# Kernel tuning notes

Measured on AMD Instinct MI355X. Metric: run time of the kernel, lower is better.

## Reference

```python
import jax, jax.numpy as jnp
import numpy as np

BATCH = 256
SEQ_LEN = 512
INPUT_DIM = 1
NUM_HIDDEN = 2048
NUM_CLASSES = 10


def _xavier(key, shape):
    fan_out, fan_in = shape
    limit = np.sqrt(6.0 / (fan_in + fan_out)).astype(np.float32)
    return jax.random.uniform(key, shape, jnp.float32, -limit, limit)


def setup_inputs() -> dict:
    key = jax.random.key(0)
    kx, k1, k2, k3 = jax.random.split(key, 4)
    x = jax.random.normal(kx, (BATCH, SEQ_LEN), jnp.float32)
    wph = _xavier(k1, (NUM_CLASSES, NUM_HIDDEN))
    whh = _xavier(k2, (NUM_HIDDEN, NUM_HIDDEN))
    whx = _xavier(k3, (NUM_HIDDEN, INPUT_DIM))
    bh = jnp.zeros((NUM_HIDDEN,), jnp.float32)
    bp = jnp.zeros((NUM_CLASSES,), jnp.float32)
    return {"x": x, "whx": whx, "whh": whh, "bh": bh, "wph": wph, "bp": bp}


def reference(x, whx, whh, bh, wph, bp):
    # x: [B, T] of scalar inputs (input_dim == 1)
    B = x.shape[0]
    H = whh.shape[0]
    whx_vec = whx[:, 0]  # [H]

    def step(h, xt):
        # xt: [B];  xt[:, None] @ whx.T  ==  outer(xt, whx_vec)
        h_new = jnp.tanh(xt[:, None] * whx_vec[None, :] + h @ whh.T + bh)
        return h_new, None

    h0 = jnp.zeros((B, H), x.dtype)
    h_last, _ = jax.lax.scan(step, h0, x.T)  # scan over time: [T, B]
    p = h_last @ wph.T + bp  # [B, num_classes]
    return p
```

## Files before the change

kernel.cpp:

```cpp
#include <hip/hip_runtime.h>

#define SEQL   512
#define HID    2048
#define NCLS   10

typedef _Float16 f16x8 __attribute__((ext_vector_type(8)));
typedef float    f32x4 __attribute__((ext_vector_type(4)));

__device__ __forceinline__ float fast_tanh(float v) {
    float e = __expf(2.0f * v);
    return 1.0f - 2.0f / (e + 1.0f);
}

__global__ void pack_w_kernel(const float* __restrict__ w, _Float16* __restrict__ o) {
    const int fid = blockIdx.x * 256 + threadIdx.x;
    int col, k0;
    if (fid < 262144) {
        const int m = fid >> 13, s5 = fid & 8191;
        const int tile = s5 >> 12, kst = (s5 >> 6) & 63, ln = s5 & 63;
        col = m * 64 + tile * 16 + (ln & 15);
        k0  = kst * 32 + (ln >> 4) * 8;
    } else {
        const int q = fid - 262144;
        const int m = q >> 13, r = q & 8191;
        const int j = r >> 10, f = (r >> 6) & 15, ln = r & 63;
        col = m * 64 + 32 + (j & 1) * 16 + (ln & 15);
        k0  = ((j >> 1) * 16 + f) * 32 + (ln >> 4) * 8;
    }
    const float* src = w + (size_t)col * HID + k0;
    f16x8 v;
    #pragma unroll
    for (int i = 0; i < 8; ++i) v[i] = (_Float16)src[i];
    *(f16x8*)(o + (size_t)fid * 8) = v;
}

__global__ void __launch_bounds__(512, 2)
rnn_main(const float* __restrict__ x, const float* __restrict__ whx,
         const _Float16* __restrict__ Wp, const float* __restrict__ bh,
         const float* __restrict__ wph, const float* __restrict__ bp,
         _Float16* __restrict__ h0, _Float16* __restrict__ h1,
         unsigned* __restrict__ ctr, float* __restrict__ out)
{
    __shared__ uint4 ldsW[8192];
    __shared__ f32x4 ldsR[16 * 64];
    __shared__ unsigned s_mslot;

    const int tid = threadIdx.x;

    int xcc;
    asm volatile("s_getreg_b32 %0, hwreg(HW_REG_XCC_ID)" : "=s"(xcc));
    const int g = xcc & 7;
    unsigned* alloc = ctr + g * 64;
    unsigned* flgA  = ctr + 512 + g * 1024;
    unsigned* flgB  = ctr + 512 + 8192 + g * 1024;
    if (tid == 0)
        s_mslot = __hip_atomic_fetch_add(alloc, 1u, __ATOMIC_RELAXED, __HIP_MEMORY_SCOPE_WORKGROUP);
    __syncthreads();
    const int m = (int)s_mslot;
    unsigned* myflgA = flgA + m * 32;
    unsigned* myflgB = flgB + m * 32;
    const int rowbase = g * 32;
    const int colbase = m * 64;

    const int lane = tid & 63;
    const int j    = tid >> 6;
    const int cbb  = j & 1;
    const int kq   = j >> 1;

    const uint4* P4 = (const uint4*)Wp;

    for (int s5 = tid; s5 < 8192; s5 += 512)
        ldsW[s5] = P4[m * 8192 + s5];

    for (int i = tid; i < 32 * 64; i += 512) {
        const int r = i >> 6, c = i & 63;
        const int b = rowbase + r, jj = colbase + c;
        h0[(size_t)b * HID + jj] = (_Float16)fast_tanh(x[(size_t)b * SEQL] * whx[jj] + bh[jj]);
    }

    const uint4* R4 = P4 + 262144 + m * 8192 + j * 1024 + lane;
    f16x8 bR[16];
    #pragma unroll
    for (int f = 0; f < 16; ++f) bR[f] = *(const f16x8*)&R4[f * 64];

    const int tj   = (j < 4) ? j : j - 4;
    const int ecls = tj >> 1, ecbb = tj & 1;
    const int ecol = colbase + ecls * 32 + ecbb * 16 + (lane & 15);
    const float wxc = whx[ecol], bbc = bh[ecol];
    const int eroff = (lane >> 4) * 4;
    const int rdbase = tj * 4;

    const size_t aoffA = (size_t)(rowbase + (lane & 15)) * HID + kq * 512 + (lane >> 4) * 8;
    const size_t aoffB = aoffA + (size_t)16 * HID;
    const uint4* bl = &ldsW[cbb * 4096 + kq * 1024 + lane];
    const unsigned* pollA = flgA + (lane & 31) * 32;
    const unsigned* pollB = flgB + (lane & 31) * 32;

    __syncthreads();
    if (tid == 0) {
        __hip_atomic_fetch_add(myflgA, 4u, __ATOMIC_RELAXED, __HIP_MEMORY_SCOPE_WORKGROUP);
        __hip_atomic_fetch_add(myflgB, 4u, __ATOMIC_RELAXED, __HIP_MEMORY_SCOPE_WORKGROUP);
    }

    for (int t = 1; t < SEQL; ++t) {
        const _Float16* hs = (t & 1) ? h0 : h1;
        _Float16*       hd = (t & 1) ? h1 : h0;
        const unsigned tgt = 4u * (unsigned)t;

        #pragma unroll
        for (int f = 0; f < 16; ++f) asm volatile("" : "+v"(bR[f]));

        {
            float xv[4];
            if (j < 4) {
                #pragma unroll
                for (int r = 0; r < 4; ++r)
                    xv[r] = x[(size_t)(rowbase + eroff + r) * SEQL + t];
            }
            unsigned v;
            do {
                v = __hip_atomic_load(pollA, __ATOMIC_RELAXED, __HIP_MEMORY_SCOPE_AGENT);
            } while (!__all((int)(v >= tgt)));
            asm volatile("buffer_inv sc0" ::: "memory");

            f16x8 av[16];
            #pragma unroll
            for (int f = 0; f < 16; ++f)
                av[f] = *(const f16x8*)(hs + aoffA + f * 32);

            f32x4 aL = {0.f,0.f,0.f,0.f}, aR = aL;
            #pragma unroll
            for (int f = 0; f < 16; ++f) {
                const f16x8 bLf = *(const f16x8*)&bl[f * 64];
                aL = __builtin_amdgcn_mfma_f32_16x16x32_f16(av[f], bLf,   aL, 0, 0, 0);
                aR = __builtin_amdgcn_mfma_f32_16x16x32_f16(av[f], bR[f], aR, 0, 0, 0);
            }

            __syncthreads();
            ldsR[(cbb * 4 + kq) * 64 + lane]       = aL;
            ldsR[((2 + cbb) * 4 + kq) * 64 + lane] = aR;
            __syncthreads();

            if (j < 4) {
                const f32x4 s = ldsR[(rdbase + 0) * 64 + lane] + ldsR[(rdbase + 1) * 64 + lane]
                              + ldsR[(rdbase + 2) * 64 + lane] + ldsR[(rdbase + 3) * 64 + lane];
                #pragma unroll
                for (int r = 0; r < 4; ++r) {
                    const int br = rowbase + eroff + r;
                    hd[(size_t)br * HID + ecol] =
                        (_Float16)fast_tanh(s[r] + xv[r] * wxc + bbc);
                }
                asm volatile("s_waitcnt vmcnt(0)" ::: "memory");
                if (lane == 0)
                    __hip_atomic_fetch_add(myflgA, 1u, __ATOMIC_RELAXED, __HIP_MEMORY_SCOPE_WORKGROUP);
            }
        }

        {
            float xv[4];
            if (j >= 4) {
                #pragma unroll
                for (int r = 0; r < 4; ++r)
                    xv[r] = x[(size_t)(rowbase + 16 + eroff + r) * SEQL + t];
            }
            unsigned v;
            do {
                v = __hip_atomic_load(pollB, __ATOMIC_RELAXED, __HIP_MEMORY_SCOPE_AGENT);
            } while (!__all((int)(v >= tgt)));
            asm volatile("buffer_inv sc0" ::: "memory");

            f16x8 av[16];
            #pragma unroll
            for (int f = 0; f < 16; ++f)
                av[f] = *(const f16x8*)(hs + aoffB + f * 32);

            f32x4 aL = {0.f,0.f,0.f,0.f}, aR = aL;
            #pragma unroll
            for (int f = 0; f < 16; ++f) {
                const f16x8 bLf = *(const f16x8*)&bl[f * 64];
                aL = __builtin_amdgcn_mfma_f32_16x16x32_f16(av[f], bLf,   aL, 0, 0, 0);
                aR = __builtin_amdgcn_mfma_f32_16x16x32_f16(av[f], bR[f], aR, 0, 0, 0);
            }

            __syncthreads();
            ldsR[(cbb * 4 + kq) * 64 + lane]       = aL;
            ldsR[((2 + cbb) * 4 + kq) * 64 + lane] = aR;
            __syncthreads();

            if (j >= 4) {
                const f32x4 s = ldsR[(rdbase + 0) * 64 + lane] + ldsR[(rdbase + 1) * 64 + lane]
                              + ldsR[(rdbase + 2) * 64 + lane] + ldsR[(rdbase + 3) * 64 + lane];
                #pragma unroll
                for (int r = 0; r < 4; ++r) {
                    const int br = rowbase + 16 + eroff + r;
                    hd[(size_t)br * HID + ecol] =
                        (_Float16)fast_tanh(s[r] + xv[r] * wxc + bbc);
                }
                asm volatile("s_waitcnt vmcnt(0)" ::: "memory");
                if (lane == 0)
                    __hip_atomic_fetch_add(myflgB, 1u, __ATOMIC_RELAXED, __HIP_MEMORY_SCOPE_WORKGROUP);
            }
        }
    }

    {
        const unsigned tgt = 4u * (unsigned)SEQL;
        unsigned v;
        do {
            v = __hip_atomic_load(pollA, __ATOMIC_RELAXED, __HIP_MEMORY_SCOPE_AGENT);
        } while (!__all((int)(v >= tgt)));
        do {
            v = __hip_atomic_load(pollB, __ATOMIC_RELAXED, __HIP_MEMORY_SCOPE_AGENT);
        } while (!__all((int)(v >= tgt)));
    }
    asm volatile("buffer_inv sc0" ::: "memory");

    const int brow = rowbase + m;
    const _Float16* hp = h1 + (size_t)brow * HID + lane * 32;
    for (int c = j; c < NCLS; c += 8) {
        const float* wp = wph + (size_t)c * HID + lane * 32;
        float psum = 0.f;
        #pragma unroll
        for (int i = 0; i < 32; ++i) psum += (float)hp[i] * wp[i];
        #pragma unroll
        for (int off = 32; off >= 1; off >>= 1) psum += __shfl_xor(psum, off, 64);
        if (lane == 0) out[brow * NCLS + c] = psum + bp[c];
    }
}

extern "C" void kernel_launch(void* const* d_in, const int* in_sizes, int n_in,
                              void* d_out, int out_size, void* d_ws, size_t ws_size,
                              hipStream_t stream) {
    const float* x   = (const float*)d_in[0];
    const float* whx = (const float*)d_in[1];
    const float* whh = (const float*)d_in[2];
    const float* bh  = (const float*)d_in[3];
    const float* wph = (const float*)d_in[4];
    const float* bp  = (const float*)d_in[5];
    float* out = (float*)d_out;

    char* ws = (char*)d_ws;
    _Float16* Wp  = (_Float16*)ws;
    _Float16* h0  = (_Float16*)(ws + (size_t)(8u << 20));
    _Float16* h1  = (_Float16*)(ws + (size_t)(9u << 20));
    unsigned* ctr = (unsigned*)(ws + (size_t)(10u << 20));

    hipMemsetAsync(ctr, 0, (512 + 2 * 8 * 1024) * sizeof(unsigned), stream);
    pack_w_kernel<<<dim3(2048), dim3(256), 0, stream>>>(whh, Wp);

    void* args[] = { (void*)&x, (void*)&whx, (void*)&Wp, (void*)&bh, (void*)&wph,
                     (void*)&bp, (void*)&h0, (void*)&h1, (void*)&ctr, (void*)&out };
    hipLaunchCooperativeKernel((const void*)rnn_main, dim3(256), dim3(512),
                               args, 0, stream);
}
```

Measured before the change: 4.380 ms.

## Give each wave full-K ownership of a column tile to drop LDS reduction

```diff
diff --git a/kernel.cpp b/kernel.cpp
--- a/kernel.cpp
+++ b/kernel.cpp
@@ -14,19 +14,14 @@
 
 __global__ void pack_w_kernel(const float* __restrict__ w, _Float16* __restrict__ o) {
     const int fid = blockIdx.x * 256 + threadIdx.x;
-    int col, k0;
-    if (fid < 262144) {
-        const int m = fid >> 13, s5 = fid & 8191;
-        const int tile = s5 >> 12, kst = (s5 >> 6) & 63, ln = s5 & 63;
-        col = m * 64 + tile * 16 + (ln & 15);
-        k0  = kst * 32 + (ln >> 4) * 8;
-    } else {
-        const int q = fid - 262144;
-        const int m = q >> 13, r = q & 8191;
-        const int j = r >> 10, f = (r >> 6) & 15, ln = r & 63;
-        col = m * 64 + 32 + (j & 1) * 16 + (ln & 15);
-        k0  = ((j >> 1) * 16 + f) * 32 + (ln >> 4) * 8;
-    }
+    const int q   = fid & 262143;
+    const int m  = q >> 13;
+    const int r13 = q & 8191;
+    const int j  = r13 >> 11;
+    const int f  = (r13 >> 6) & 31;
+    const int ln = r13 & 63;
+    const int col = m * 64 + j * 16 + (ln & 15);
+    const int k0  = ((fid < 262144 ? 0 : 32) + f) * 32 + (ln >> 4) * 8;
     const float* src = w + (size_t)col * HID + k0;
     f16x8 v;
     #pragma unroll
@@ -34,15 +29,14 @@
     *(f16x8*)(o + (size_t)fid * 8) = v;
 }
 
-__global__ void __launch_bounds__(512, 2)
+__global__ void __launch_bounds__(256, 1)
 rnn_main(const float* __restrict__ x, const float* __restrict__ whx,
          const _Float16* __restrict__ Wp, const float* __restrict__ bh,
          const float* __restrict__ wph, const float* __restrict__ bp,
          _Float16* __restrict__ h0, _Float16* __restrict__ h1,
          unsigned* __restrict__ ctr, float* __restrict__ out)
 {
-    __shared__ uint4 ldsW[8192];
-    __shared__ f32x4 ldsR[16 * 64];
+    __shared__ uint4 ldsB[8192];
     __shared__ unsigned s_mslot;
 
     const int tid = threadIdx.x;
@@ -64,35 +58,29 @@
 
     const int lane = tid & 63;
     const int j    = tid >> 6;
-    const int cbb  = j & 1;
-    const int kq   = j >> 1;
 
     const uint4* P4 = (const uint4*)Wp;
 
-    for (int s5 = tid; s5 < 8192; s5 += 512)
-        ldsW[s5] = P4[m * 8192 + s5];
-
-    for (int i = tid; i < 32 * 64; i += 512) {
+    for (int s5 = tid; s5 < 8192; s5 += 256)
+        ldsB[s5] = P4[262144 + m * 8192 + s5];
+
+    for (int i = tid; i < 32 * 64; i += 256) {
         const int r = i >> 6, c = i & 63;
         const int b = rowbase + r, jj = colbase + c;
         h0[(size_t)b * HID + jj] = (_Float16)fast_tanh(x[(size_t)b * SEQL] * whx[jj] + bh[jj]);
     }
 
-    const uint4* R4 = P4 + 262144 + m * 8192 + j * 1024 + lane;
-    f16x8 bR[16];
+    const uint4* R4 = P4 + m * 8192 + j * 2048 + lane;
+    f16x8 bReg[32];
     #pragma unroll
-    for (int f = 0; f < 16; ++f) bR[f] = *(const f16x8*)&R4[f * 64];
-
-    const int tj   = (j < 4) ? j : j - 4;
-    const int ecls = tj >> 1, ecbb = tj & 1;
-    const int ecol = colbase + ecls * 32 + ecbb * 16 + (lane & 15);
+    for (int f = 0; f < 32; ++f) bReg[f] = *(const f16x8*)&R4[f * 64];
+
+    const int ecol = colbase + j * 16 + (lane & 15);
     const float wxc = whx[ecol], bbc = bh[ecol];
     const int eroff = (lane >> 4) * 4;
-    const int rdbase = tj * 4;
-
-    const size_t aoffA = (size_t)(rowbase + (lane & 15)) * HID + kq * 512 + (lane >> 4) * 8;
+    const size_t aoffA = (size_t)(rowbase + (lane & 15)) * HID + (lane >> 4) * 8;
     const size_t aoffB = aoffA + (size_t)16 * HID;
-    const uint4* bl = &ldsW[cbb * 4096 + kq * 1024 + lane];
+    const uint4* bl = &ldsB[j * 2048 + lane];
     const unsigned* pollA = flgA + (lane & 31) * 32;
     const unsigned* pollB = flgB + (lane & 31) * 32;
 
@@ -108,98 +96,74 @@
         const unsigned tgt = 4u * (unsigned)t;
 
         #pragma unroll
-        for (int f = 0; f < 16; ++f) asm volatile("" : "+v"(bR[f]));
+        for (int f = 0; f < 32; ++f) asm volatile("" : "+v"(bReg[f]));
 
         {
             float xv[4];
-            if (j < 4) {
-                #pragma unroll
-                for (int r = 0; r < 4; ++r)
-                    xv[r] = x[(size_t)(rowbase + eroff + r) * SEQL + t];
-            }
+            #pragma unroll
+            for (int r = 0; r < 4; ++r)
+                xv[r] = x[(size_t)(rowbase + eroff + r) * SEQL + t];
+
             unsigned v;
             do {
                 v = __hip_atomic_load(pollA, __ATOMIC_RELAXED, __HIP_MEMORY_SCOPE_AGENT);
             } while (!__all((int)(v >= tgt)));
             asm volatile("buffer_inv sc0" ::: "memory");
 
-            f16x8 av[16];
-            #pragma unroll
-            for (int f = 0; f < 16; ++f)
-                av[f] = *(const f16x8*)(hs + aoffA + f * 32);
-
-            f32x4 aL = {0.f,0.f,0.f,0.f}, aR = aL;
-            #pragma unroll
-            for (int f = 0; f < 16; ++f) {
-                const f16x8 bLf = *(const f16x8*)&bl[f * 64];
-                aL = __builtin_amdgcn_mfma_f32_16x16x32_f16(av[f], bLf,   aL, 0, 0, 0);
-                aR = __builtin_amdgcn_mfma_f32_16x16x32_f16(av[f], bR[f], aR, 0, 0, 0);
-            }
-
-            __syncthreads();
-            ldsR[(cbb * 4 + kq) * 64 + lane]       = aL;
-            ldsR[((2 + cbb) * 4 + kq) * 64 + lane] = aR;
-            __syncthreads();
-
-            if (j < 4) {
-                const f32x4 s = ldsR[(rdbase + 0) * 64 + lane] + ldsR[(rdbase + 1) * 64 + lane]
-                              + ldsR[(rdbase + 2) * 64 + lane] + ldsR[(rdbase + 3) * 64 + lane];
-                #pragma unroll
-                for (int r = 0; r < 4; ++r) {
-                    const int br = rowbase + eroff + r;
-                    hd[(size_t)br * HID + ecol] =
-                        (_Float16)fast_tanh(s[r] + xv[r] * wxc + bbc);
-                }
-                asm volatile("s_waitcnt vmcnt(0)" ::: "memory");
-                if (lane == 0)
-                    __hip_atomic_fetch_add(myflgA, 1u, __ATOMIC_RELAXED, __HIP_MEMORY_SCOPE_WORKGROUP);
-            }
+            const _Float16* ap = hs + aoffA;
+            f32x4 accR = {0.f,0.f,0.f,0.f}, accL = accR;
+            #pragma unroll
+            for (int f = 0; f < 32; ++f) {
+                const f16x8 aR_ = *(const f16x8*)(ap + f * 32);
+                const f16x8 aL_ = *(const f16x8*)(ap + 1024 + f * 32);
+                const f16x8 bL_ = *(const f16x8*)&bl[f * 64];
+                accR = __builtin_amdgcn_mfma_f32_16x16x32_f16(aR_, bReg[f], accR, 0, 0, 0);
+                accL = __builtin_amdgcn_mfma_f32_16x16x32_f16(aL_, bL_,     accL, 0, 0, 0);
+            }
+            const f32x4 s = accR + accL;
+            #pragma unroll
+            for (int r = 0; r < 4; ++r) {
+                const int br = rowbase + eroff + r;
+                hd[(size_t)br * HID + ecol] =
+                    (_Float16)fast_tanh(s[r] + xv[r] * wxc + bbc);
+            }
+            asm volatile("s_waitcnt vmcnt(0)" ::: "memory");
+            if (lane == 0)
+                __hip_atomic_fetch_add(myflgA, 1u, __ATOMIC_RELAXED, __HIP_MEMORY_SCOPE_WORKGROUP);
         }
 
         {
             float xv[4];
-            if (j >= 4) {
-                #pragma unroll
-                for (int r = 0; r < 4; ++r)
-                    xv[r] = x[(size_t)(rowbase + 16 + eroff + r) * SEQL + t];
-            }
+            #pragma unroll
+            for (int r = 0; r < 4; ++r)
+                xv[r] = x[(size_t)(rowbase + 16 + eroff + r) * SEQL + t];
+
             unsigned v;
             do {
                 v = __hip_atomic_load(pollB, __ATOMIC_RELAXED, __HIP_MEMORY_SCOPE_AGENT);
             } while (!__all((int)(v >= tgt)));
             asm volatile("buffer_inv sc0" ::: "memory");
 
-            f16x8 av[16];
-            #pragma unroll
-            for (int f = 0; f < 16; ++f)
-                av[f] = *(const f16x8*)(hs + aoffB + f * 32);
-
-            f32x4 aL = {0.f,0.f,0.f,0.f}, aR = aL;
-            #pragma unroll
-            for (int f = 0; f < 16; ++f) {
-                const f16x8 bLf = *(const f16x8*)&bl[f * 64];
-                aL = __builtin_amdgcn_mfma_f32_16x16x32_f16(av[f], bLf,   aL, 0, 0, 0);
-                aR = __builtin_amdgcn_mfma_f32_16x16x32_f16(av[f], bR[f], aR, 0, 0, 0);
-            }
-
-            __syncthreads();
-            ldsR[(cbb * 4 + kq) * 64 + lane]       = aL;
-            ldsR[((2 + cbb) * 4 + kq) * 64 + lane] = aR;
-            __syncthreads();
-
-            if (j >= 4) {
-                const f32x4 s = ldsR[(rdbase + 0) * 64 + lane] + ldsR[(rdbase + 1) * 64 + lane]
-                              + ldsR[(rdbase + 2) * 64 + lane] + ldsR[(rdbase + 3) * 64 + lane];
-                #pragma unroll
-                for (int r = 0; r < 4; ++r) {
-                    const int br = rowbase + 16 + eroff + r;
-                    hd[(size_t)br * HID + ecol] =
-                        (_Float16)fast_tanh(s[r] + xv[r] * wxc + bbc);
-                }
-                asm volatile("s_waitcnt vmcnt(0)" ::: "memory");
-                if (lane == 0)
-                    __hip_atomic_fetch_add(myflgB, 1u, __ATOMIC_RELAXED, __HIP_MEMORY_SCOPE_WORKGROUP);
-            }
+            const _Float16* ap = hs + aoffB;
+            f32x4 accR = {0.f,0.f,0.f,0.f}, accL = accR;
+            #pragma unroll
+            for (int f = 0; f < 32; ++f) {
+                const f16x8 aR_ = *(const f16x8*)(ap + f * 32);
+                const f16x8 aL_ = *(const f16x8*)(ap + 1024 + f * 32);
+                const f16x8 bL_ = *(const f16x8*)&bl[f * 64];
+                accR = __builtin_amdgcn_mfma_f32_16x16x32_f16(aR_, bReg[f], accR, 0, 0, 0);
+                accL = __builtin_amdgcn_mfma_f32_16x16x32_f16(aL_, bL_,     accL, 0, 0, 0);
+            }
+            const f32x4 s = accR + accL;
+            #pragma unroll
+            for (int r = 0; r < 4; ++r) {
+                const int br = rowbase + 16 + eroff + r;
+                hd[(size_t)br * HID + ecol] =
+                    (_Float16)fast_tanh(s[r] + xv[r] * wxc + bbc);
+            }
+            asm volatile("s_waitcnt vmcnt(0)" ::: "memory");
+            if (lane == 0)
+                __hip_atomic_fetch_add(myflgB, 1u, __ATOMIC_RELAXED, __HIP_MEMORY_SCOPE_WORKGROUP);
         }
     }
 
@@ -217,7 +181,7 @@
 
     const int brow = rowbase + m;
     const _Float16* hp = h1 + (size_t)brow * HID + lane * 32;
-    for (int c = j; c < NCLS; c += 8) {
+    for (int c = j; c < NCLS; c += 4) {
         const float* wp = wph + (size_t)c * HID + lane * 32;
         float psum = 0.f;
         #pragma unroll
@@ -250,6 +214,6 @@
 
     void* args[] = { (void*)&x, (void*)&whx, (void*)&Wp, (void*)&bh, (void*)&wph,
                      (void*)&bp, (void*)&h0, (void*)&h1, (void*)&ctr, (void*)&out };
-    hipLaunchCooperativeKernel((const void*)rnn_main, dim3(256), dim3(512),
+    hipLaunchCooperativeKernel((const void*)rnn_main, dim3(256), dim3(256),
                                args, 0, stream);
 }
```

New measurement: 7.907 ms. 1.81x slower.
